# Kernel optimization log

Measured on AMD Instinct MI355X. Metric: run time of the kernel, lower is better.

The kernel has to match this reference:

```python
import jax, jax.numpy as jnp
import numpy as np

NUM_HEADS = 4
SPLIT = 2
DIM_FULL = 384  # constructor dim; scale uses dim // num_heads
SCALE = (DIM_FULL // NUM_HEADS) ** -0.5


def img2windows(img, ws, nh):
    # img: (B, D, H, W, C) -> (num_windows, nh, N, C//nh), N = prod(ws)
    B, D, H, W, C = img.shape
    d, h, w = ws
    x = img.reshape(B, D // d, d, H // h, h, W // w, w, C)
    x = x.transpose(0, 1, 3, 5, 2, 4, 6, 7).reshape(-1, d * h * w, C)
    return x.reshape(-1, d * h * w, nh, C // nh).transpose(0, 2, 1, 3)


def windows2img(xw, ws, B, D, H, W):
    # xw: (num_windows, d, h, w, C) -> (B, D, H, W, C)
    d, h, w = ws
    x = xw.reshape(B, D // d, H // h, W // w, d, h, w, -1)
    return x.transpose(0, 1, 4, 2, 5, 3, 6, 7).reshape(B, D, H, W, -1)


def setup_inputs() -> dict:
    key = jax.random.key(0)
    ks = jax.random.split(key, 5)
    B, D, H, W, C = 2, 8, 64, 64, 96
    qkv = jax.random.normal(ks[0], (3, B, D, H, W, C), jnp.float32)
    conv_w = jax.random.normal(ks[1], (C, 1, 3, 3, 3), jnp.float32) * 0.1  # depthwise Conv3d weight (O, I/groups, kD, kH, kW)
    conv_b = jax.random.normal(ks[2], (C,), jnp.float32) * 0.01
    proj_w = jax.random.normal(ks[3], (C, C), jnp.float32) * (C ** -0.5)  # torch Linear weight (out, in)
    proj_b = jax.random.normal(ks[4], (C,), jnp.float32) * 0.01
    return {"qkv": qkv, "conv_w": conv_w, "conv_b": conv_b, "proj_w": proj_w, "proj_b": proj_b}


def reference(qkv, conv_w, conv_b, proj_w, proj_b):
    q, k, v = qkv[0], qkv[1], qkv[2]
    B, D, H, W, C = q.shape
    ws = (1, H, SPLIT)  # idx == 0: (D_sp, H_sp, W_sp) = (1, H, split_size)
    qw = img2windows(q, ws, NUM_HEADS) * SCALE  # (nw, nh, N, hd)
    kw = img2windows(k, ws, NUM_HEADS)
    vw = img2windows(v, ws, NUM_HEADS)
    # LePE: depthwise 3x3x3 conv over v in NCDHW layout
    x = v.transpose(0, 4, 1, 2, 3)
    lepe = jax.lax.conv_general_dilated(
        x, conv_w, window_strides=(1, 1, 1), padding=[(1, 1)] * 3,
        dimension_numbers=("NCDHW", "OIDHW", "NCDHW"),
        feature_group_count=C) + conv_b[None, :, None, None, None]
    lepe = lepe.transpose(0, 2, 3, 4, 1)
    lepew = img2windows(lepe, ws, NUM_HEADS)
    # per-window attention
    attn = jax.nn.softmax(jnp.einsum("whnd,whmd->whnm", qw, kw), axis=-1)
    out = jnp.einsum("whnm,whmd->whnd", attn, vw) + lepew  # (nw, nh, N, hd)
    N = qw.shape[2]
    out = out.transpose(0, 2, 1, 3).reshape(-1, N, C)
    out = out @ proj_w.T + proj_b
    out = out.reshape(-1, ws[0], ws[1], ws[2], C)
    return windows2img(out, ws, B, D, H, W)
```

## Files before the change

### kernel.cpp

```cpp
#include <hip/hip_runtime.h>
#include <hip/hip_bf16.h>

constexpr int D_ = 8, H_ = 64, W_ = 64, C_ = 96;
constexpr int WC    = W_ * C_;
constexpr int HWC   = H_ * W_ * C_;
constexpr int BDHWC = 2 * D_ * HWC;
constexpr float SCALE = 0.10206207261596577f;

typedef __attribute__((ext_vector_type(4))) float f32x4;
typedef __attribute__((ext_vector_type(8))) short s16x8;

__device__ inline ushort f2bf(float x) {
  union { __hip_bfloat16 h; ushort u; } c;
  c.h = __float2bfloat16(x);
  return c.u;
}
__device__ inline float bf2f(ushort u) {
  union { float f; unsigned i; } c;
  c.i = ((unsigned)u) << 16;
  return c.f;
}
__device__ inline int xswz8(int bid, int nwg) {
  return (bid & 7) * (nwg >> 3) + (bid >> 3);
}

constexpr int QSTR  = 40;
constexpr int PSTR  = 136;
constexpr int PSTR2 = 72;

__global__ void __launch_bounds__(256, 4)
attn_mfma_kernel(const float* __restrict__ qkv, float* __restrict__ out) {
  __shared__ ushort sK[128 * QSTR];
  __shared__ ushort sVt[32 * PSTR];
  __shared__ ushort sP[128 * PSTR2];

  const int t    = threadIdx.x;
  const int bid  = xswz8(blockIdx.x, 2048);
  const int head = bid & 3;
  const int nw   = bid >> 2;
  const int wq   = nw & 31;
  const int d    = (nw >> 5) & 7;
  const int b    = nw >> 8;
  const int hc   = head * 24;

  const float* qpl = qkv + (size_t)(b * 8 + d) * HWC;
  const float* kpl = qpl + BDHWC;
  const float* vpl = kpl + BDHWC;

  {
    const s16x8 Z = {0, 0, 0, 0, 0, 0, 0, 0};
    int row = t >> 1, col = 24 + (t & 1) * 8;
    *reinterpret_cast<s16x8*>(&sK[row * QSTR + col]) = Z;
    if (t < 136) *reinterpret_cast<s16x8*>(&sVt[24 * PSTR + t * 8]) = Z;
  }

  #pragma unroll
  for (int it = 0; it < 3; ++it) {
    int idx = t + it * 256;
    int tok = idx / 6, c4 = (idx - tok * 6) * 4;
    int g = (tok >> 1) * WC + (wq * 2 + (tok & 1)) * 96 + hc + c4;
    float4 kv = *reinterpret_cast<const float4*>(kpl + g);
    float4 vv = *reinterpret_cast<const float4*>(vpl + g);
    ushort4 kh = { f2bf(kv.x), f2bf(kv.y), f2bf(kv.z), f2bf(kv.w) };
    *reinterpret_cast<ushort4*>(&sK[tok * QSTR + c4]) = kh;
    sVt[(c4 + 0) * PSTR + tok] = f2bf(vv.x);
    sVt[(c4 + 1) * PSTR + tok] = f2bf(vv.y);
    sVt[(c4 + 2) * PSTR + tok] = f2bf(vv.z);
    sVt[(c4 + 3) * PSTR + tok] = f2bf(vv.w);
  }

  const int wv = t >> 6, lane = t & 63;
  const int lr = lane & 15;
  const int lg = lane >> 4;
  const int r0 = (2 * wv) * 16;
  const int r1 = (2 * wv + 1) * 16;

  s16x8 a0 = {0,0,0,0,0,0,0,0}, a1 = {0,0,0,0,0,0,0,0};
  if (lg < 3) {
    union { s16x8 v; ushort u[8]; } qa;
    int tok = r0 + lr;
    const float* qp = qpl + (tok >> 1) * WC + (wq * 2 + (tok & 1)) * 96 + hc + lg * 8;
    float4 x0 = *reinterpret_cast<const float4*>(qp);
    float4 x1 = *reinterpret_cast<const float4*>(qp + 4);
    qa.u[0] = f2bf(x0.x * SCALE); qa.u[1] = f2bf(x0.y * SCALE);
    qa.u[2] = f2bf(x0.z * SCALE); qa.u[3] = f2bf(x0.w * SCALE);
    qa.u[4] = f2bf(x1.x * SCALE); qa.u[5] = f2bf(x1.y * SCALE);
    qa.u[6] = f2bf(x1.z * SCALE); qa.u[7] = f2bf(x1.w * SCALE);
    a0 = qa.v;
    tok = r1 + lr;
    qp = qpl + (tok >> 1) * WC + (wq * 2 + (tok & 1)) * 96 + hc + lg * 8;
    x0 = *reinterpret_cast<const float4*>(qp);
    x1 = *reinterpret_cast<const float4*>(qp + 4);
    qa.u[0] = f2bf(x0.x * SCALE); qa.u[1] = f2bf(x0.y * SCALE);
    qa.u[2] = f2bf(x0.z * SCALE); qa.u[3] = f2bf(x0.w * SCALE);
    qa.u[4] = f2bf(x1.x * SCALE); qa.u[5] = f2bf(x1.y * SCALE);
    qa.u[6] = f2bf(x1.z * SCALE); qa.u[7] = f2bf(x1.w * SCALE);
    a1 = qa.v;
  }

  __syncthreads();

  float rsum[2][4];
  #pragma unroll
  for (int rb = 0; rb < 2; ++rb)
    #pragma unroll
    for (int r = 0; r < 4; ++r) rsum[rb][r] = 0.f;

  f32x4 accO[2][2];
  #pragma unroll
  for (int i = 0; i < 2; ++i)
    #pragma unroll
    for (int j = 0; j < 2; ++j) accO[i][j] = f32x4{0.f, 0.f, 0.f, 0.f};

  #pragma unroll
  for (int half = 0; half < 2; ++half) {
    f32x4 accS[2][4];
    #pragma unroll
    for (int i = 0; i < 2; ++i)
      #pragma unroll
      for (int j = 0; j < 4; ++j) accS[i][j] = f32x4{0.f, 0.f, 0.f, 0.f};

    #pragma unroll
    for (int nb = 0; nb < 4; ++nb) {
      s16x8 bb = *reinterpret_cast<const s16x8*>(
          &sK[(half * 64 + nb * 16 + lr) * QSTR + lg * 8]);
      accS[0][nb] = __builtin_amdgcn_mfma_f32_16x16x32_bf16(a0, bb, accS[0][nb], 0, 0, 0);
      accS[1][nb] = __builtin_amdgcn_mfma_f32_16x16x32_bf16(a1, bb, accS[1][nb], 0, 0, 0);
    }

    #pragma unroll
    for (int rb = 0; rb < 2; ++rb)
      #pragma unroll
      for (int nb = 0; nb < 4; ++nb)
        #pragma unroll
        for (int r = 0; r < 4; ++r) {
          float e = __expf(accS[rb][nb][r]);
          accS[rb][nb][r] = e;
          rsum[rb][r] += e;
        }

    if (half) __syncthreads();

    #pragma unroll
    for (int rb = 0; rb < 2; ++rb)
      #pragma unroll
      for (int nb = 0; nb < 4; ++nb)
        #pragma unroll
        for (int r = 0; r < 4; ++r)
          sP[((2 * wv + rb) * 16 + lg * 4 + r) * PSTR2 + nb * 16 + lr] =
              f2bf(accS[rb][nb][r]);
    __syncthreads();

    #pragma unroll
    for (int kb = 0; kb < 2; ++kb) {
      int kc = half * 64 + kb * 32 + lg * 8;
      s16x8 pa0 = *reinterpret_cast<const s16x8*>(&sP[(r0 + lr) * PSTR2 + kb * 32 + lg * 8]);
      s16x8 pa1 = *reinterpret_cast<const s16x8*>(&sP[(r1 + lr) * PSTR2 + kb * 32 + lg * 8]);
      s16x8 vb0 = *reinterpret_cast<const s16x8*>(&sVt[lr * PSTR + kc]);
      s16x8 vb1 = *reinterpret_cast<const s16x8*>(&sVt[(16 + lr) * PSTR + kc]);
      accO[0][0] = __builtin_amdgcn_mfma_f32_16x16x32_bf16(pa0, vb0, accO[0][0], 0, 0, 0);
      accO[0][1] = __builtin_amdgcn_mfma_f32_16x16x32_bf16(pa0, vb1, accO[0][1], 0, 0, 0);
      accO[1][0] = __builtin_amdgcn_mfma_f32_16x16x32_bf16(pa1, vb0, accO[1][0], 0, 0, 0);
      accO[1][1] = __builtin_amdgcn_mfma_f32_16x16x32_bf16(pa1, vb1, accO[1][1], 0, 0, 0);
    }
  }

  float* opl = out + (size_t)(b * 8 + d) * HWC;
  #pragma unroll
  for (int rb = 0; rb < 2; ++rb) {
    #pragma unroll
    for (int r = 0; r < 4; ++r) {
      float s = rsum[rb][r];
      s += __shfl_xor(s, 1); s += __shfl_xor(s, 2);
      s += __shfl_xor(s, 4); s += __shfl_xor(s, 8);
      int tok = (2 * wv + rb) * 16 + lg * 4 + r;
      int g = (tok >> 1) * WC + (wq * 2 + (tok & 1)) * 96 + hc;
      float inv = 1.0f / s;
      opl[g + lr] = accO[rb][0][r] * inv;
      if (lr < 8) opl[g + 16 + lr] = accO[rb][1][r] * inv;
    }
  }
}

constexpr int VSTR = 104;
constexpr int WSTR = 104;

__global__ void __launch_bounds__(256, 4)
lepe_proj_fused_kernel(const float* __restrict__ qkv, const float* __restrict__ cw,
                       const float* __restrict__ cbias, const float* __restrict__ pw,
                       const float* __restrict__ pb, float* __restrict__ io) {
  __shared__ ushort sV[64 * VSTR];
  __shared__ ushort sW[96 * WSTR];
  __shared__ ushort sCW[27 * 96];
  __shared__ float  sCB[96];
  __shared__ float  sPB[96];

  const int t   = threadIdx.x;
  const int bid = xswz8(blockIdx.x, 1024);
  const int h   = bid & 63;
  const int d   = (bid >> 6) & 7;
  const int b   = bid >> 9;

  float* iop = io + (size_t)(b * 8 + d) * HWC + h * WC;
  const float* vbatch = qkv + 2 * (size_t)BDHWC + (size_t)b * 8 * HWC;

  const int tt  = t >> 2;
  const int cbk = (t & 3) * 24;

  float4 az[6];
  #pragma unroll
  for (int j = 0; j < 6; ++j)
    az[j] = *reinterpret_cast<const float4*>(iop + tt * 96 + cbk + j * 4);

  #pragma unroll
  for (int it = 0; it < 9; ++it) {
    int idx = t + it * 256;
    int co = idx / 24, c4 = (idx - co * 24) * 4;
    float4 x = *reinterpret_cast<const float4*>(pw + co * 96 + c4);
    ushort4 hx = { f2bf(x.x), f2bf(x.y), f2bf(x.z), f2bf(x.w) };
    *reinterpret_cast<ushort4*>(&sW[co * WSTR + c4]) = hx;
  }
  for (int idx = t; idx < 2592; idx += 256) {
    int c = idx / 27, tap = idx - c * 27;
    sCW[tap * 96 + c] = f2bf(cw[idx]);
  }
  if (t < 96) { sCB[t] = cbias[t]; sPB[t] = pb[t]; }

  float lep[24];
  #pragma unroll
  for (int j = 0; j < 6; ++j) {
    lep[4*j+0] = az[j].x; lep[4*j+1] = az[j].y;
    lep[4*j+2] = az[j].z; lep[4*j+3] = az[j].w;
  }

  const float fw0 = (tt > 0)  ? 1.f : 0.f;
  const float fw2 = (tt < 63) ? 1.f : 0.f;
  const int   zw0 = (tt > 0)  ? tt - 1 : 0;
  const int   zw2 = (tt < 63) ? tt + 1 : 63;

  #define TAP(zw, tap, FW)                                                   \
    {                                                                        \
      _Pragma("unroll")                                                      \
      for (int j8 = 0; j8 < 3; ++j8) {                                       \
        union { s16x8 v; ushort u[8]; } vu;                                  \
        vu.v = *reinterpret_cast<const s16x8*>(&sV[(zw) * VSTR + cbk + j8 * 8]); \
        union { s16x8 v; ushort u[8]; } wu;                                  \
        wu.v = *reinterpret_cast<const s16x8*>(&sCW[(tap) * 96 + cbk + j8 * 8]); \
        _Pragma("unroll")                                                    \
        for (int e = 0; e < 8; ++e)                                          \
          lep[8*j8+e] = fmaf(bf2f(vu.u[e]) * (FW), bf2f(wu.u[e]), lep[8*j8+e]); \
      }                                                                      \
    }

  #pragma unroll
  for (int dd = 0; dd < 3; ++dd) {
    int zd = d + dd - 1;
    if (zd < 0 || zd >= D_) continue;
    #pragma unroll
    for (int dh = 0; dh < 3; ++dh) {
      int zh = h + dh - 1;
      if (zh < 0 || zh >= H_) continue;
      __syncthreads();
      {
        const float4* src = reinterpret_cast<const float4*>(
            vbatch + (size_t)zd * HWC + zh * WC);
        #pragma unroll
        for (int it = 0; it < 6; ++it) {
          int idx = t + it * 256;
          int tok = idx / 24, c4 = idx - tok * 24;
          float4 x = src[idx];
          ushort4 hx = { f2bf(x.x), f2bf(x.y), f2bf(x.z), f2bf(x.w) };
          *reinterpret_cast<ushort4*>(&sV[tok * VSTR + c4 * 4]) = hx;
        }
      }
      __syncthreads();
      const int tap0 = dd * 9 + dh * 3;
      TAP(zw0, tap0 + 0, fw0);
      TAP(tt,  tap0 + 1, 1.f);
      TAP(zw2, tap0 + 2, fw2);
    }
  }
  #undef TAP

  __syncthreads();
  #pragma unroll
  for (int j = 0; j < 6; ++j) {
    float4 bz = *reinterpret_cast<const float4*>(sCB + cbk + j * 4);
    ushort4 hx = { f2bf(lep[4*j+0] + bz.x), f2bf(lep[4*j+1] + bz.y),
                   f2bf(lep[4*j+2] + bz.z), f2bf(lep[4*j+3] + bz.w) };
    *reinterpret_cast<ushort4*>(&sV[tt * VSTR + cbk + j * 4]) = hx;
  }
  __syncthreads();

  const int wv = t >> 6, lane = t & 63;
  const int lr = lane & 15, lg = lane >> 4;

  f32x4 acc[6];
  #pragma unroll
  for (int cb = 0; cb < 6; ++cb) {
    float bv = sPB[cb * 16 + lr];
    acc[cb] = f32x4{bv, bv, bv, bv};
  }
  s16x8 afr[3];
  #pragma unroll
  for (int kb = 0; kb < 3; ++kb)
    afr[kb] = *reinterpret_cast<const s16x8*>(&sV[(wv * 16 + lr) * VSTR + kb * 32 + lg * 8]);
  #pragma unroll
  for (int kb = 0; kb < 3; ++kb) {
    #pragma unroll
    for (int cb = 0; cb < 6; ++cb) {
      s16x8 bfr = *reinterpret_cast<const s16x8*>(&sW[(cb * 16 + lr) * WSTR + kb * 32 + lg * 8]);
      acc[cb] = __builtin_amdgcn_mfma_f32_16x16x32_bf16(afr[kb], bfr, acc[cb], 0, 0, 0);
    }
  }

  #pragma unroll
  for (int cb = 0; cb < 6; ++cb) {
    #pragma unroll
    for (int r = 0; r < 4; ++r) {
      int tok = wv * 16 + lg * 4 + r;
      iop[tok * 96 + cb * 16 + lr] = acc[cb][r];
    }
  }
}

extern "C" void kernel_launch(void* const* d_in, const int* in_sizes, int n_in,
                              void* d_out, int out_size, void* d_ws, size_t ws_size,
                              hipStream_t stream) {
  const float* qkv = (const float*)d_in[0];
  const float* cw  = (const float*)d_in[1];
  const float* cb  = (const float*)d_in[2];
  const float* pw  = (const float*)d_in[3];
  const float* pb  = (const float*)d_in[4];
  float* out = (float*)d_out;

  hipLaunchKernelGGL(attn_mfma_kernel, dim3(2048), dim3(256), 0, stream, qkv, out);
  hipLaunchKernelGGL(lepe_proj_fused_kernel, dim3(1024), dim3(256), 0, stream,
                     qkv, cw, cb, pw, pb, out);
}
```

Baseline: 62.03 us.

## Pass attention output via bf16 workspace and prefetch LePE rows into registers

The attention kernel now writes its per-head output as bf16 into the workspace buffer, and the fused LePE/projection kernel reads it from there, halving that intermediate traffic when the workspace is large enough. The LePE loop also switches to register double-buffering: the next neighbour row is loaded into registers while the current one is converted into shared memory and convolved, and out-of-range taps are skipped through loop bounds. Rounding the intermediate to bf16 costs some accuracy. The fallback path keeps the fp32 route through the output buffer.

```diff
diff --git a/kernel.cpp b/kernel.cpp
--- a/kernel.cpp
+++ b/kernel.cpp
@@ -28,8 +28,10 @@
 constexpr int PSTR  = 136;
 constexpr int PSTR2 = 72;
 
+template <bool WSOUT>
 __global__ void __launch_bounds__(256, 4)
-attn_mfma_kernel(const float* __restrict__ qkv, float* __restrict__ out) {
+attn_mfma_kernel(const float* __restrict__ qkv, float* __restrict__ out,
+                 ushort* __restrict__ ws) {
   __shared__ ushort sK[128 * QSTR];
   __shared__ ushort sVt[32 * PSTR];
   __shared__ ushort sP[128 * PSTR2];
@@ -165,7 +167,8 @@
     }
   }
 
-  float* opl = out + (size_t)(b * 8 + d) * HWC;
+  float* opl   = out + (size_t)(b * 8 + d) * HWC;
+  ushort* wpl  = ws  + (size_t)(b * 8 + d) * HWC;
   #pragma unroll
   for (int rb = 0; rb < 2; ++rb) {
     #pragma unroll
@@ -176,8 +179,13 @@
       int tok = (2 * wv + rb) * 16 + lg * 4 + r;
       int g = (tok >> 1) * WC + (wq * 2 + (tok & 1)) * 96 + hc;
       float inv = 1.0f / s;
-      opl[g + lr] = accO[rb][0][r] * inv;
-      if (lr < 8) opl[g + 16 + lr] = accO[rb][1][r] * inv;
+      if (WSOUT) {
+        wpl[g + lr] = f2bf(accO[rb][0][r] * inv);
+        if (lr < 8) wpl[g + 16 + lr] = f2bf(accO[rb][1][r] * inv);
+      } else {
+        opl[g + lr] = accO[rb][0][r] * inv;
+        if (lr < 8) opl[g + 16 + lr] = accO[rb][1][r] * inv;
+      }
     }
   }
 }
@@ -185,10 +193,12 @@
 constexpr int VSTR = 104;
 constexpr int WSTR = 104;
 
+template <bool WSIN>
 __global__ void __launch_bounds__(256, 4)
 lepe_proj_fused_kernel(const float* __restrict__ qkv, const float* __restrict__ cw,
                        const float* __restrict__ cbias, const float* __restrict__ pw,
-                       const float* __restrict__ pb, float* __restrict__ io) {
+                       const float* __restrict__ pb, float* __restrict__ io,
+                       const ushort* __restrict__ ws) {
   __shared__ ushort sV[64 * VSTR];
   __shared__ ushort sW[96 * WSTR];
   __shared__ ushort sCW[27 * 96];
@@ -202,15 +212,33 @@
   const int b   = bid >> 9;
 
   float* iop = io + (size_t)(b * 8 + d) * HWC + h * WC;
+  const ushort* wsp = ws + (size_t)(b * 8 + d) * HWC + h * WC;
   const float* vbatch = qkv + 2 * (size_t)BDHWC + (size_t)b * 8 * HWC;
 
   const int tt  = t >> 2;
   const int cbk = (t & 3) * 24;
 
-  float4 az[6];
-  #pragma unroll
-  for (int j = 0; j < 6; ++j)
-    az[j] = *reinterpret_cast<const float4*>(iop + tt * 96 + cbk + j * 4);
+  float lep[24];
+  if (WSIN) {
+    union { s16x8 v; ushort u[8]; } azu[3];
+    #pragma unroll
+    for (int k = 0; k < 3; ++k)
+      azu[k].v = *reinterpret_cast<const s16x8*>(wsp + tt * 96 + cbk + k * 8);
+    #pragma unroll
+    for (int k = 0; k < 3; ++k)
+      #pragma unroll
+      for (int e = 0; e < 8; ++e) lep[8*k+e] = bf2f(azu[k].u[e]);
+  } else {
+    float4 az[6];
+    #pragma unroll
+    for (int j = 0; j < 6; ++j)
+      az[j] = *reinterpret_cast<const float4*>(iop + tt * 96 + cbk + j * 4);
+    #pragma unroll
+    for (int j = 0; j < 6; ++j) {
+      lep[4*j+0] = az[j].x; lep[4*j+1] = az[j].y;
+      lep[4*j+2] = az[j].z; lep[4*j+3] = az[j].w;
+    }
+  }
 
   #pragma unroll
   for (int it = 0; it < 9; ++it) {
@@ -225,13 +253,6 @@
     sCW[tap * 96 + c] = f2bf(cw[idx]);
   }
   if (t < 96) { sCB[t] = cbias[t]; sPB[t] = pb[t]; }
-
-  float lep[24];
-  #pragma unroll
-  for (int j = 0; j < 6; ++j) {
-    lep[4*j+0] = az[j].x; lep[4*j+1] = az[j].y;
-    lep[4*j+2] = az[j].z; lep[4*j+3] = az[j].w;
-  }
 
   const float fw0 = (tt > 0)  ? 1.f : 0.f;
   const float fw2 = (tt < 63) ? 1.f : 0.f;
@@ -252,35 +273,47 @@
       }                                                                      \
     }
 
-  #pragma unroll
-  for (int dd = 0; dd < 3; ++dd) {
-    int zd = d + dd - 1;
-    if (zd < 0 || zd >= D_) continue;
-    #pragma unroll
-    for (int dh = 0; dh < 3; ++dh) {
-      int zh = h + dh - 1;
-      if (zh < 0 || zh >= H_) continue;
-      __syncthreads();
-      {
-        const float4* src = reinterpret_cast<const float4*>(
-            vbatch + (size_t)zd * HWC + zh * WC);
-        #pragma unroll
-        for (int it = 0; it < 6; ++it) {
-          int idx = t + it * 256;
-          int tok = idx / 24, c4 = idx - tok * 24;
-          float4 x = src[idx];
-          ushort4 hx = { f2bf(x.x), f2bf(x.y), f2bf(x.z), f2bf(x.w) };
-          *reinterpret_cast<ushort4*>(&sV[tok * VSTR + c4 * 4]) = hx;
-        }
+  const int dd_lo = (d == 0) ? 1 : 0, dd_hi = (d == 7) ? 1 : 2;
+  const int dh_lo = (h == 0) ? 1 : 0, dh_hi = (h == 63) ? 1 : 2;
+
+  float4 pf[6];
+  #define LOADR(zd, zh)                                                      \
+    {                                                                        \
+      const float4* src = reinterpret_cast<const float4*>(                   \
+          vbatch + (size_t)(zd) * HWC + (zh) * WC);                          \
+      _Pragma("unroll")                                                      \
+      for (int k = 0; k < 6; ++k) pf[k] = src[t + k * 256];                  \
+    }
+
+  LOADR(d + dd_lo - 1, h + dh_lo - 1);
+
+  int i = 0;
+  const int ntot = (dd_hi - dd_lo + 1) * (dh_hi - dh_lo + 1);
+  for (int dd = dd_lo; dd <= dd_hi; ++dd) {
+    for (int dh = dh_lo; dh <= dh_hi; ++dh) {
+      if (i) __syncthreads();
+      #pragma unroll
+      for (int k = 0; k < 6; ++k) {
+        int idx = t + k * 256;
+        int tok = idx / 24, c4 = idx - tok * 24;
+        ushort4 hx = { f2bf(pf[k].x), f2bf(pf[k].y), f2bf(pf[k].z), f2bf(pf[k].w) };
+        *reinterpret_cast<ushort4*>(&sV[tok * VSTR + c4 * 4]) = hx;
+      }
+      if (i + 1 < ntot) {
+        int nd = (dh < dh_hi) ? dd : dd + 1;
+        int nh = (dh < dh_hi) ? dh + 1 : dh_lo;
+        LOADR(d + nd - 1, h + nh - 1);
       }
       __syncthreads();
       const int tap0 = dd * 9 + dh * 3;
       TAP(zw0, tap0 + 0, fw0);
       TAP(tt,  tap0 + 1, 1.f);
       TAP(zw2, tap0 + 2, fw2);
+      ++i;
     }
   }
   #undef TAP
+  #undef LOADR
 
   __syncthreads();
   #pragma unroll
@@ -333,8 +366,18 @@
   const float* pw  = (const float*)d_in[3];
   const float* pb  = (const float*)d_in[4];
   float* out = (float*)d_out;
-
-  hipLaunchKernelGGL(attn_mfma_kernel, dim3(2048), dim3(256), 0, stream, qkv, out);
-  hipLaunchKernelGGL(lepe_proj_fused_kernel, dim3(1024), dim3(256), 0, stream,
-                     qkv, cw, cb, pw, pb, out);
-}
+  ushort* ws = (ushort*)d_ws;
+
+  const size_t need = (size_t)2 * D_ * HWC * sizeof(ushort);
+  if (ws_size >= need) {
+    hipLaunchKernelGGL((attn_mfma_kernel<true>), dim3(2048), dim3(256), 0, stream,
+                       qkv, out, ws);
+    hipLaunchKernelGGL((lepe_proj_fused_kernel<true>), dim3(1024), dim3(256), 0, stream,
+                       qkv, cw, cb, pw, pb, out, ws);
+  } else {
+    hipLaunchKernelGGL((attn_mfma_kernel<false>), dim3(2048), dim3(256), 0, stream,
+                       qkv, out, ws);
+    hipLaunchKernelGGL((lepe_proj_fused_kernel<false>), dim3(1024), dim3(256), 0, stream,
+                       qkv, cw, cb, pw, pb, out, ws);
+  }
+}
```

After: 72.24 us. 16.5% more time.
